# Kernel tuning notes

Measured on AMD Instinct MI355X. Metric: run time of the kernel, lower is better.

The kernel has to match this reference:

```python
import jax, jax.numpy as jnp
import numpy as np

NUM_GRAPHS = 256


def _gcn_norm(edge_index, num_nodes):
    # Add self-loops and compute symmetric normalization coeffs (PyG gcn_norm).
    loops = jnp.arange(num_nodes, dtype=edge_index.dtype)
    row = jnp.concatenate([edge_index[0], loops])  # source nodes
    col = jnp.concatenate([edge_index[1], loops])  # target nodes
    deg = jax.ops.segment_sum(jnp.ones_like(col, dtype=jnp.float32), col,
                              num_segments=num_nodes)
    dis = jnp.where(deg > 0, jax.lax.rsqrt(jnp.maximum(deg, 1.0)), 0.0)
    norm = dis[row] * dis[col]  # [E + N]
    return row, col, norm


def _gcn_conv(x, row, col, norm, W, b, num_nodes):
    h = x @ W                                        # [N, out] dense transform first
    msg = norm[:, None] * h[row]                     # gather + scale  [E+N, out]
    out = jax.ops.segment_sum(msg, col, num_segments=num_nodes)  # scatter-add
    return out + b


def setup_inputs() -> dict:
    key = jax.random.key(0)
    k = jax.random.split(key, 12)
    N, E, F_IN, H = 100000, 1600000, 64, 64
    x = jax.random.normal(k[0], (N, F_IN), dtype=jnp.float32)
    edge_index = jax.random.randint(k[1], (2, E), 0, N, dtype=jnp.int64)
    batch_index = jnp.sort(jax.random.randint(k[2], (N,), 0, NUM_GRAPHS, dtype=jnp.int64))
    s = 1.0 / np.sqrt(F_IN)
    W1 = jax.random.uniform(k[3], (F_IN, H), minval=-s, maxval=s, dtype=jnp.float32)
    b1 = jnp.zeros((H,), dtype=jnp.float32)
    W2 = jax.random.uniform(k[4], (H, H), minval=-s, maxval=s, dtype=jnp.float32)
    b2 = jnp.zeros((H,), dtype=jnp.float32)
    Wl1 = jax.random.uniform(k[5], (H, H // 2), minval=-s, maxval=s, dtype=jnp.float32)
    bl1 = jax.random.uniform(k[6], (H // 2,), minval=-s, maxval=s, dtype=jnp.float32)
    Wl2 = jax.random.uniform(k[7], (H // 2, 2), minval=-s, maxval=s, dtype=jnp.float32)
    bl2 = jax.random.uniform(k[8], (2,), minval=-s, maxval=s, dtype=jnp.float32)
    return {"x": x, "edge_index": edge_index, "batch_index": batch_index,
            "W1": W1, "b1": b1, "W2": W2, "b2": b2,
            "Wl1": Wl1, "bl1": bl1, "Wl2": Wl2, "bl2": bl2}


def reference(x, edge_index, batch_index, W1, b1, W2, b2, Wl1, bl1, Wl2, bl2):
    N = x.shape[0]
    row, col, norm = _gcn_norm(edge_index, N)
    h = jax.nn.relu(_gcn_conv(x, row, col, norm, W1, b1, N))
    h = jax.nn.relu(_gcn_conv(h, row, col, norm, W2, b2, N))
    # global mean pool over batch_index
    sums = jax.ops.segment_sum(h, batch_index, num_segments=NUM_GRAPHS)
    cnts = jax.ops.segment_sum(jnp.ones((N,), dtype=h.dtype), batch_index,
                               num_segments=NUM_GRAPHS)
    g = sums / jnp.maximum(cnts, 1.0)[:, None]       # [G, H]
    g = jax.nn.relu(g @ Wl1 + bl1)                    # dropout is identity in eval
    logits = g @ Wl2 + bl2
    return jax.nn.log_softmax(logits, axis=1)
```

## Files before the change

### kernel.cpp

```cpp
#include <hip/hip_runtime.h>
#include <hip/hip_fp8.h>
#include <cstdint>
#include <cstddef>


#define HF 64
#define BSH 8
#define BSZ 256
#define PCHUNK 4096
#define PADB 6144
#define CNTCLAMP (PADB - 4 * BSZ)
#define POISON 0xAAAAAAAAu

typedef unsigned u32;

__device__ __forceinline__ unsigned short f2bf(float x) {
    unsigned u = __float_as_uint(x);
    unsigned r = (u + 0x7fffu + ((u >> 16) & 1u)) >> 16;
    return (unsigned short)r;
}
__device__ __forceinline__ float bfl(u32 w) { return __uint_as_float(w << 16); }
__device__ __forceinline__ float bfh(u32 w) { return __uint_as_float(w & 0xffff0000u); }

__device__ __forceinline__ u32 pack_fp8x4(float a, float b, float c, float d) {
#if __has_builtin(__builtin_amdgcn_cvt_pk_fp8_f32)
    int v = 0;
    v = __builtin_amdgcn_cvt_pk_fp8_f32(a, b, v, false);
    v = __builtin_amdgcn_cvt_pk_fp8_f32(c, d, v, true);
    return (u32)v;
#else
    __hip_fp8_e4m3 fa(a), fb(b), fc(c), fd(d);
    return (u32)fa.__x | ((u32)fb.__x << 8) | ((u32)fc.__x << 16) | ((u32)fd.__x << 24);
#endif
}
__device__ __forceinline__ void acc_fp8x4(float4& acc, u32 w) {
#if __has_builtin(__builtin_amdgcn_cvt_pk_f32_fp8)
    typedef float v2f __attribute__((ext_vector_type(2)));
    v2f lo = __builtin_amdgcn_cvt_pk_f32_fp8((int)w, false);
    v2f hi = __builtin_amdgcn_cvt_pk_f32_fp8((int)w, true);
    acc.x += lo[0]; acc.y += lo[1]; acc.z += hi[0]; acc.w += hi[1];
#else
    __hip_fp8_e4m3 a, b, c, d;
    a.__x = (unsigned char)(w);       b.__x = (unsigned char)(w >> 8);
    c.__x = (unsigned char)(w >> 16); d.__x = (unsigned char)(w >> 24);
    acc.x += (float)a; acc.y += (float)b; acc.z += (float)c; acc.w += (float)d;
#endif
}

__global__ __launch_bounds__(256) void k_part(const int* __restrict__ rows,
                                              const int* __restrict__ cols,
                                              u32* __restrict__ gcurb,
                                              u32* __restrict__ part, int E) {
    __shared__ u32 hist[512];
    __shared__ u32 off[512];
    __shared__ u32 obase[512];
    __shared__ u32 cur[512];
    __shared__ u32 sc[256];
    __shared__ u32 stage[PCHUNK];
    __shared__ unsigned short sbk[PCHUNK];
    const int tid = threadIdx.x;
    const int e0  = blockIdx.x * PCHUNK;
    u32 er[16], ec[16];

    hist[tid] = 0; hist[tid + 256] = 0;
    __syncthreads();
#pragma unroll
    for (int j = 0; j < 16; ++j) {
        int e = e0 + j * 256 + tid;
        if (e < E) {
            ec[j] = (u32)cols[e];
            er[j] = (u32)rows[e];
            atomicAdd(&hist[ec[j] >> BSH], 1u);
        } else ec[j] = 0xFFFFFFFFu;
    }
    __syncthreads();
    u32 c0 = hist[2 * tid], c1 = hist[2 * tid + 1];
    u32 s = c0 + c1;
    sc[tid] = s;
    __syncthreads();
    for (int o = 1; o < 256; o <<= 1) {
        u32 t = (tid >= o) ? sc[tid - o] : 0u;
        __syncthreads();
        sc[tid] += t;
        __syncthreads();
    }
    u32 ex = sc[tid] - s;
    off[2 * tid] = ex;          cur[2 * tid] = ex;
    off[2 * tid + 1] = ex + c0; cur[2 * tid + 1] = ex + c0;
    obase[2 * tid]     = c0 ? (atomicAdd(&gcurb[2 * tid], c0) - POISON) : 0u;
    obase[2 * tid + 1] = c1 ? (atomicAdd(&gcurb[2 * tid + 1], c1) - POISON) : 0u;
    __syncthreads();
#pragma unroll
    for (int j = 0; j < 16; ++j) {
        if (ec[j] != 0xFFFFFFFFu) {
            u32 bk  = ec[j] >> BSH;
            u32 pos = atomicAdd(&cur[bk], 1u);
            stage[pos] = ((ec[j] & (BSZ - 1)) << 17) | er[j];
            sbk[pos]   = (unsigned short)bk;
        }
    }
    __syncthreads();
    const int total = (e0 + PCHUNK <= E) ? PCHUNK : (E - e0);
    for (int i = tid; i < total; i += 256) {
        u32 bk = sbk[i];
        u32 pb = obase[bk] + ((u32)i - off[bk]);
        if (pb < PADB)
            part[(size_t)bk * PADB + pb] = stage[i];
    }
}

__global__ __launch_bounds__(256) void k_place2(const u32* __restrict__ gcurb,
                                                const u32* __restrict__ part,
                                                const float* __restrict__ x,
                                                u32* __restrict__ rowptr,
                                                float* __restrict__ dis,
                                                u32* __restrict__ s08,
                                                u32* __restrict__ h18,
                                                int* __restrict__ eidx,
                                                int N, float S0) {
    __shared__ u32 cnt_[256];
    __shared__ u32 off_[257];
    __shared__ u32 sc[256];
    __shared__ u32 cur[256];
    __shared__ u32 outb[PADB];
    const int tid = threadIdx.x;
    const int b   = blockIdx.x;
    const int n0  = b << BSH;
    const u32 base = (u32)b * PADB;
    u32 cntB = gcurb[b] - POISON; if (cntB > CNTCLAMP) cntB = CNTCLAMP;

    if (b == 0 && tid < 16) {
        s08[(size_t)N * 16 + tid] = 0u;
        h18[(size_t)N * 16 + tid] = 0u;
    }

    cnt_[tid] = 0;
    __syncthreads();
    for (u32 i = tid; i < cntB; i += 256)
        atomicAdd(&cnt_[part[base + i] >> 17], 1u);
    __syncthreads();
    u32 v  = cnt_[tid];
    bool live = (n0 + tid) < N;
    u32 vs = v + 1u;
    u32 p  = live ? ((vs + 3u) & ~3u) : 0u;
    sc[tid] = p;
    __syncthreads();
    for (int o = 1; o < 256; o <<= 1) {
        u32 t = (tid >= o) ? sc[tid - o] : 0u;
        __syncthreads();
        sc[tid] += t;
        __syncthreads();
    }
    u32 ex = sc[tid] - p;
    off_[tid] = ex; cur[tid] = ex;
    if (tid == 255) off_[256] = sc[255];
    __syncthreads();
    const u32 cntP = off_[256];
    if (live) {
        u32 dg = vs; if (dg > 1023u) dg = 1023u;
        rowptr[n0 + tid] = (base + ex) | (dg << 22);
        dis[n0 + tid]    = rsqrtf(1.0f + (float)v);
    }
    {
        int nmax = min(256, N - n0);
        for (int idx = tid; idx < nmax * 16; idx += 256) {
            int nl = idx >> 4, f4 = idx & 15;
            float d  = S0 * rsqrtf(1.0f + (float)cnt_[nl]);
            float4 xv = ((const float4*)(x + (size_t)(n0 + nl) * HF))[f4];
            s08[(size_t)(n0 + nl) * 16 + f4] =
                pack_fp8x4(d * xv.x, d * xv.y, d * xv.z, d * xv.w);
        }
    }
    for (u32 i = tid; i < cntP; i += 256) outb[i] = (u32)N;
    __syncthreads();
    for (u32 i = tid; i < cntB; i += 256) {
        u32 pv  = part[base + i];
        u32 pos = atomicAdd(&cur[pv >> 17], 1u);
        outb[pos] = pv & 0x1FFFFu;
    }
    __syncthreads();
    if (live) outb[cur[tid]] = (u32)tid;
    __syncthreads();
    for (u32 i = tid; i < cntP; i += 256)
        eidx[base + i] = (int)outb[i];
}

template <int OUTFP8>
__global__ __launch_bounds__(256, 4) void k_gtrans(const u32* __restrict__ rowptr,
                                                   const int* __restrict__ eidx,
                                                   const u32* __restrict__ hs8,
                                                   const float* __restrict__ W,
                                                   const float* __restrict__ dis,
                                                   const float* __restrict__ bias,
                                                   void* __restrict__ OUTp, int N,
                                                   float invS, float outS) {
    __shared__ float ws[64 * 64];
    __shared__ float xs[64 * 68];
    const int tid  = threadIdx.x;
    const int row0 = blockIdx.x * 64;

#pragma unroll
    for (int i = 0; i < 4; ++i) {
        int idx4 = i * 256 + tid;
        *(float4*)&ws[idx4 * 4] = ((const float4*)W)[idx4];
    }

    const int qq = tid >> 4;
    const int f4 = tid & 15;
#pragma unroll 1
    for (int j = 0; j < 4; ++j) {
        const int n = row0 + qq * 4 + j;
        float4 acc = float4{0.f, 0.f, 0.f, 0.f};
        if (n < N) {
            u32 rp    = rowptr[n];
            u32 start = rp & 0x3FFFFFu;
            int ngr   = (int)(((rp >> 22) + 3u) >> 2);
            const uint4* eb = (const uint4*)(eidx + start);
            int g = 0;
            for (; g + 1 < ngr; g += 2) {
                uint4 ea = eb[g];
                uint4 eb2 = eb[g + 1];
                u32 wa0 = hs8[(size_t)ea.x * 16 + f4];
                u32 wa1 = hs8[(size_t)ea.y * 16 + f4];
                u32 wa2 = hs8[(size_t)ea.z * 16 + f4];
                u32 wa3 = hs8[(size_t)ea.w * 16 + f4];
                u32 wb0 = hs8[(size_t)eb2.x * 16 + f4];
                u32 wb1 = hs8[(size_t)eb2.y * 16 + f4];
                u32 wb2 = hs8[(size_t)eb2.z * 16 + f4];
                u32 wb3 = hs8[(size_t)eb2.w * 16 + f4];
                acc_fp8x4(acc, wa0); acc_fp8x4(acc, wa1);
                acc_fp8x4(acc, wa2); acc_fp8x4(acc, wa3);
                acc_fp8x4(acc, wb0); acc_fp8x4(acc, wb1);
                acc_fp8x4(acc, wb2); acc_fp8x4(acc, wb3);
            }
            if (g < ngr) {
                uint4 ea = eb[g];
                u32 w0 = hs8[(size_t)ea.x * 16 + f4];
                u32 w1 = hs8[(size_t)ea.y * 16 + f4];
                u32 w2 = hs8[(size_t)ea.z * 16 + f4];
                u32 w3 = hs8[(size_t)ea.w * 16 + f4];
                acc_fp8x4(acc, w0); acc_fp8x4(acc, w1);
                acc_fp8x4(acc, w2); acc_fp8x4(acc, w3);
            }
        }
        *(float4*)&xs[(qq * 4 + j) * 68 + f4 * 4] = acc;
    }
    __syncthreads();

    const int rg = tid >> 4;
    const int cg = tid & 15;
    float4 a0 = float4{0.f, 0.f, 0.f, 0.f};
    float4 a1 = a0, a2 = a0, a3 = a0;

#pragma unroll 8
    for (int k = 0; k < 64; ++k) {
        float4 wv = *(float4*)&ws[k * 64 + cg * 4];
        float  x0 = xs[(rg * 4 + 0) * 68 + k];
        float  x1 = xs[(rg * 4 + 1) * 68 + k];
        float  x2 = xs[(rg * 4 + 2) * 68 + k];
        float  x3 = xs[(rg * 4 + 3) * 68 + k];
        a0.x += x0 * wv.x; a0.y += x0 * wv.y; a0.z += x0 * wv.z; a0.w += x0 * wv.w;
        a1.x += x1 * wv.x; a1.y += x1 * wv.y; a1.z += x1 * wv.z; a1.w += x1 * wv.w;
        a2.x += x2 * wv.x; a2.y += x2 * wv.y; a2.z += x2 * wv.z; a2.w += x2 * wv.w;
        a3.x += x3 * wv.x; a3.y += x3 * wv.y; a3.z += x3 * wv.z; a3.w += x3 * wv.w;
    }

    float4 bv = ((const float4*)bias)[cg];
    float4 accs[4] = {a0, a1, a2, a3};
#pragma unroll
    for (int j = 0; j < 4; ++j) {
        int row = row0 + rg * 4 + j;
        if (row < N) {
            float d  = dis[row];
            float dd = d * invS;
            float4 a = accs[j];
            a.x = fmaxf(dd * a.x + bv.x, 0.f);
            a.y = fmaxf(dd * a.y + bv.y, 0.f);
            a.z = fmaxf(dd * a.z + bv.z, 0.f);
            a.w = fmaxf(dd * a.w + bv.w, 0.f);
            if (OUTFP8) {
                float so = d * outS;
                ((u32*)OUTp)[(size_t)row * 16 + cg] =
                    pack_fp8x4(so * a.x, so * a.y, so * a.z, so * a.w);
            } else {
                ushort4 pk;
                pk.x = f2bf(a.x); pk.y = f2bf(a.y);
                pk.z = f2bf(a.z); pk.w = f2bf(a.w);
                *(ushort4*)&((unsigned short*)OUTp)[(size_t)row * HF + cg * 4] = pk;
            }
        }
    }
}

__device__ __forceinline__ int lower_bound(const int* __restrict__ a, int n, int key) {
    int lo = 0, hi = n;
    while (lo < hi) { int mid = (lo + hi) >> 1; if (a[mid] < key) lo = mid + 1; else hi = mid; }
    return lo;
}

__global__ __launch_bounds__(256) void k_poolhead(const u32* __restrict__ h2,
                                                  const int* __restrict__ batch,
                                                  const float* __restrict__ Wl1,
                                                  const float* __restrict__ bl1,
                                                  const float* __restrict__ Wl2,
                                                  const float* __restrict__ bl2,
                                                  float* __restrict__ out, int N) {
    __shared__ float red[4][64];
    __shared__ float gm[64];
    const int g    = blockIdx.x;
    const int lane = threadIdx.x & 63;
    const int w    = threadIdx.x >> 6;
    int s = lower_bound(batch, N, g);
    int e = lower_bound(batch, N, g + 1);
    float acc = 0.f;
    for (int n = s + w; n < e; n += 4) {
        u32 wv = h2[(size_t)n * 32 + (lane >> 1)];
        acc += (lane & 1) ? bfh(wv) : bfl(wv);
    }
    red[w][lane] = acc;
    __syncthreads();
    if (w == 0) {
        float t = red[0][lane] + red[1][lane] + red[2][lane] + red[3][lane];
        gm[lane] = t / fmaxf((float)(e - s), 1.0f);
    }
    __syncthreads();
    if (w == 0 && lane < 32) {
        float a = bl1[lane];
#pragma unroll
        for (int k = 0; k < 64; ++k) a += gm[k] * Wl1[k * 32 + lane];
        a = fmaxf(a, 0.f);
        float l0 = a * Wl2[2 * lane];
        float l1 = a * Wl2[2 * lane + 1];
#pragma unroll
        for (int o = 1; o < 32; o <<= 1) {
            l0 += __shfl_xor(l0, o);
            l1 += __shfl_xor(l1, o);
        }
        if (lane == 0) {
            l0 += bl2[0]; l1 += bl2[1];
            float m   = fmaxf(l0, l1);
            float lse = m + logf(expf(l0 - m) + expf(l1 - m));
            out[2 * g]     = l0 - lse;
            out[2 * g + 1] = l1 - lse;
        }
    }
}

extern "C" void kernel_launch(void* const* d_in, const int* in_sizes, int n_in,
                              void* d_out, int out_size, void* d_ws, size_t ws_size,
                              hipStream_t stream) {
    const float* x   = (const float*)d_in[0];
    const int*   ei  = (const int*)d_in[1];
    const int*   bi  = (const int*)d_in[2];
    const float* W1  = (const float*)d_in[3];
    const float* b1  = (const float*)d_in[4];
    const float* W2  = (const float*)d_in[5];
    const float* b2  = (const float*)d_in[6];
    const float* Wl1 = (const float*)d_in[7];
    const float* bl1 = (const float*)d_in[8];
    const float* Wl2 = (const float*)d_in[9];
    const float* bl2 = (const float*)d_in[10];
    float* out = (float*)d_out;

    const int N = in_sizes[0] / HF;
    const int E = in_sizes[1] / 2;
    const int* rows = ei;
    const int* cols = ei + E;
    const int NB = (N + BSZ - 1) / BSZ;
    const size_t EP = (size_t)NB * PADB;

    const float S0 = 4.0f, S1 = 16.0f;

    float* ws = (float*)d_ws;
    size_t o = 0;
    float* dis    = ws + o; o += ((size_t)N + 63) / 64 * 64;
    u32*   A8     = (u32*)(ws + o); o += (size_t)(N + 1) * 16;
    u32*   B8     = (u32*)(ws + o); o += (size_t)(N + 1) * 16;
    unsigned short* Cbf = (unsigned short*)(ws + o); o += (size_t)N * 32;
    u32*   rowptr = (u32*)(ws + o); o += ((size_t)N + 63) / 64 * 64;
    u32*   part   = (u32*)(ws + o); o += EP;
    int*   eidx   = (int*)(ws + o); o += EP;
    u32*   gcurb  = (u32*)(ws + o); o += 512;

    const int tb = (N + 63) / 64;

    k_part<<<(E + PCHUNK - 1) / PCHUNK, 256, 0, stream>>>(rows, cols, gcurb, part, E);
    k_place2<<<NB, 256, 0, stream>>>(gcurb, part, x, rowptr, dis, A8, B8, eidx, N, S0);

    k_gtrans<1><<<tb, 256, 0, stream>>>(rowptr, eidx, A8, W1, dis, b1, (void*)B8,
                                        N, 1.0f / S0, S1);
    k_gtrans<0><<<tb, 256, 0, stream>>>(rowptr, eidx, B8, W2, dis, b2, (void*)Cbf,
                                        N, 1.0f / S1, 0.f);

    k_poolhead<<<256, 256, 0, stream>>>((const u32*)Cbf, bi, Wl1, bl1, Wl2, bl2, out, N);
}
```

Before: 249.3 us.

## Split gather across half-waves, store aggregated rows as bf16, split pooling across blocks

The gather in k_gtrans now has two 16-lane groups process alternate edge-groups of the same node and combine their partial sums with a shuffle. The aggregated rows are stored in shared memory as packed bf16, which roughly halves that buffer and lets launch bounds rise from 4 to 6 blocks per CU. Mean pooling is split over four blocks per graph using atomic adds into a zeroed buffer, and a separate small head kernel finishes the MLP. The aim is more memory-level parallelism and occupancy. In exchange there is bf16 rounding before the dense transform, float atomics, and one extra kernel launch.

```diff
diff --git a/kernel.cpp b/kernel.cpp
--- a/kernel.cpp
+++ b/kernel.cpp
@@ -11,6 +11,7 @@
 #define PADB 6144
 #define CNTCLAMP (PADB - 4 * BSZ)
 #define POISON 0xAAAAAAAAu
+#define NG 256
 
 typedef unsigned u32;
 
@@ -117,6 +118,7 @@
                                                 u32* __restrict__ s08,
                                                 u32* __restrict__ h18,
                                                 int* __restrict__ eidx,
+                                                float* __restrict__ gm,
                                                 int N, float S0) {
     __shared__ u32 cnt_[256];
     __shared__ u32 off_[257];
@@ -133,6 +135,9 @@
         s08[(size_t)N * 16 + tid] = 0u;
         h18[(size_t)N * 16 + tid] = 0u;
     }
+    if (b == 0) {
+        for (int i = tid; i < NG * HF; i += 256) gm[i] = 0.f;
+    }
 
     cnt_[tid] = 0;
     __syncthreads();
@@ -186,7 +191,7 @@
 }
 
 template <int OUTFP8>
-__global__ __launch_bounds__(256, 4) void k_gtrans(const u32* __restrict__ rowptr,
+__global__ __launch_bounds__(256, 6) void k_gtrans(const u32* __restrict__ rowptr,
                                                    const int* __restrict__ eidx,
                                                    const u32* __restrict__ hs8,
                                                    const float* __restrict__ W,
@@ -195,7 +200,7 @@
                                                    void* __restrict__ OUTp, int N,
                                                    float invS, float outS) {
     __shared__ float ws[64 * 64];
-    __shared__ float xs[64 * 68];
+    __shared__ u32 xs2[64 * 34];
     const int tid  = threadIdx.x;
     const int row0 = blockIdx.x * 64;
 
@@ -205,45 +210,42 @@
         *(float4*)&ws[idx4 * 4] = ((const float4*)W)[idx4];
     }
 
-    const int qq = tid >> 4;
-    const int f4 = tid & 15;
+    const int wv   = tid >> 6;
+    const int lane = tid & 63;
+    const int h    = lane >> 5;
+    const int qh   = (lane >> 4) & 1;
+    const int f4   = lane & 15;
 #pragma unroll 1
-    for (int j = 0; j < 4; ++j) {
-        const int n = row0 + qq * 4 + j;
+    for (int p = 0; p < 8; ++p) {
+        const int nl = wv * 16 + 2 * p + h;
+        const int n  = row0 + nl;
         float4 acc = float4{0.f, 0.f, 0.f, 0.f};
         if (n < N) {
             u32 rp    = rowptr[n];
             u32 start = rp & 0x3FFFFFu;
             int ngr   = (int)(((rp >> 22) + 3u) >> 2);
             const uint4* eb = (const uint4*)(eidx + start);
-            int g = 0;
-            for (; g + 1 < ngr; g += 2) {
-                uint4 ea = eb[g];
-                uint4 eb2 = eb[g + 1];
-                u32 wa0 = hs8[(size_t)ea.x * 16 + f4];
-                u32 wa1 = hs8[(size_t)ea.y * 16 + f4];
-                u32 wa2 = hs8[(size_t)ea.z * 16 + f4];
-                u32 wa3 = hs8[(size_t)ea.w * 16 + f4];
-                u32 wb0 = hs8[(size_t)eb2.x * 16 + f4];
-                u32 wb1 = hs8[(size_t)eb2.y * 16 + f4];
-                u32 wb2 = hs8[(size_t)eb2.z * 16 + f4];
-                u32 wb3 = hs8[(size_t)eb2.w * 16 + f4];
-                acc_fp8x4(acc, wa0); acc_fp8x4(acc, wa1);
-                acc_fp8x4(acc, wa2); acc_fp8x4(acc, wa3);
-                acc_fp8x4(acc, wb0); acc_fp8x4(acc, wb1);
-                acc_fp8x4(acc, wb2); acc_fp8x4(acc, wb3);
-            }
-            if (g < ngr) {
-                uint4 ea = eb[g];
-                u32 w0 = hs8[(size_t)ea.x * 16 + f4];
-                u32 w1 = hs8[(size_t)ea.y * 16 + f4];
-                u32 w2 = hs8[(size_t)ea.z * 16 + f4];
-                u32 w3 = hs8[(size_t)ea.w * 16 + f4];
+#pragma unroll 1
+            for (int g = qh; g < ngr; g += 2) {
+                uint4 e4 = eb[g];
+                u32 w0 = hs8[(size_t)e4.x * 16 + f4];
+                u32 w1 = hs8[(size_t)e4.y * 16 + f4];
+                u32 w2 = hs8[(size_t)e4.z * 16 + f4];
+                u32 w3 = hs8[(size_t)e4.w * 16 + f4];
                 acc_fp8x4(acc, w0); acc_fp8x4(acc, w1);
                 acc_fp8x4(acc, w2); acc_fp8x4(acc, w3);
             }
         }
-        *(float4*)&xs[(qq * 4 + j) * 68 + f4 * 4] = acc;
+        acc.x += __shfl_xor(acc.x, 16);
+        acc.y += __shfl_xor(acc.y, 16);
+        acc.z += __shfl_xor(acc.z, 16);
+        acc.w += __shfl_xor(acc.w, 16);
+        if (qh == 0) {
+            u32 lo = (u32)f2bf(acc.x) | ((u32)f2bf(acc.y) << 16);
+            u32 hi = (u32)f2bf(acc.z) | ((u32)f2bf(acc.w) << 16);
+            xs2[nl * 34 + f4 * 2]     = lo;
+            xs2[nl * 34 + f4 * 2 + 1] = hi;
+        }
     }
     __syncthreads();
 
@@ -252,17 +254,26 @@
     float4 a0 = float4{0.f, 0.f, 0.f, 0.f};
     float4 a1 = a0, a2 = a0, a3 = a0;
 
-#pragma unroll 8
-    for (int k = 0; k < 64; ++k) {
-        float4 wv = *(float4*)&ws[k * 64 + cg * 4];
-        float  x0 = xs[(rg * 4 + 0) * 68 + k];
-        float  x1 = xs[(rg * 4 + 1) * 68 + k];
-        float  x2 = xs[(rg * 4 + 2) * 68 + k];
-        float  x3 = xs[(rg * 4 + 3) * 68 + k];
-        a0.x += x0 * wv.x; a0.y += x0 * wv.y; a0.z += x0 * wv.z; a0.w += x0 * wv.w;
-        a1.x += x1 * wv.x; a1.y += x1 * wv.y; a1.z += x1 * wv.z; a1.w += x1 * wv.w;
-        a2.x += x2 * wv.x; a2.y += x2 * wv.y; a2.z += x2 * wv.z; a2.w += x2 * wv.w;
-        a3.x += x3 * wv.x; a3.y += x3 * wv.y; a3.z += x3 * wv.z; a3.w += x3 * wv.w;
+#pragma unroll 4
+    for (int k2 = 0; k2 < 32; ++k2) {
+        float4 wv0 = *(float4*)&ws[(2 * k2)     * 64 + cg * 4];
+        float4 wv1 = *(float4*)&ws[(2 * k2 + 1) * 64 + cg * 4];
+        u32 p0 = xs2[(rg * 4 + 0) * 34 + k2];
+        u32 p1 = xs2[(rg * 4 + 1) * 34 + k2];
+        u32 p2 = xs2[(rg * 4 + 2) * 34 + k2];
+        u32 p3 = xs2[(rg * 4 + 3) * 34 + k2];
+        float x0e = bfl(p0), x0o = bfh(p0);
+        float x1e = bfl(p1), x1o = bfh(p1);
+        float x2e = bfl(p2), x2o = bfh(p2);
+        float x3e = bfl(p3), x3o = bfh(p3);
+        a0.x += x0e * wv0.x; a0.y += x0e * wv0.y; a0.z += x0e * wv0.z; a0.w += x0e * wv0.w;
+        a1.x += x1e * wv0.x; a1.y += x1e * wv0.y; a1.z += x1e * wv0.z; a1.w += x1e * wv0.w;
+        a2.x += x2e * wv0.x; a2.y += x2e * wv0.y; a2.z += x2e * wv0.z; a2.w += x2e * wv0.w;
+        a3.x += x3e * wv0.x; a3.y += x3e * wv0.y; a3.z += x3e * wv0.z; a3.w += x3e * wv0.w;
+        a0.x += x0o * wv1.x; a0.y += x0o * wv1.y; a0.z += x0o * wv1.z; a0.w += x0o * wv1.w;
+        a1.x += x1o * wv1.x; a1.y += x1o * wv1.y; a1.z += x1o * wv1.z; a1.w += x1o * wv1.w;
+        a2.x += x2o * wv1.x; a2.y += x2o * wv1.y; a2.z += x2o * wv1.z; a2.w += x2o * wv1.w;
+        a3.x += x3o * wv1.x; a3.y += x3o * wv1.y; a3.z += x3o * wv1.z; a3.w += x3o * wv1.w;
     }
 
     float4 bv = ((const float4*)bias)[cg];
@@ -298,22 +309,21 @@
     return lo;
 }
 
-__global__ __launch_bounds__(256) void k_poolhead(const u32* __restrict__ h2,
-                                                  const int* __restrict__ batch,
-                                                  const float* __restrict__ Wl1,
-                                                  const float* __restrict__ bl1,
-                                                  const float* __restrict__ Wl2,
-                                                  const float* __restrict__ bl2,
-                                                  float* __restrict__ out, int N) {
+__global__ __launch_bounds__(256) void k_pool(const u32* __restrict__ h2,
+                                              const int* __restrict__ batch,
+                                              float* __restrict__ gm, int N) {
     __shared__ float red[4][64];
-    __shared__ float gm[64];
-    const int g    = blockIdx.x;
+    const int g    = blockIdx.x >> 2;
+    const int sl   = blockIdx.x & 3;
     const int lane = threadIdx.x & 63;
     const int w    = threadIdx.x >> 6;
     int s = lower_bound(batch, N, g);
     int e = lower_bound(batch, N, g + 1);
+    int len = e - s;
+    int q0 = s + ((len * sl) >> 2);
+    int q1 = s + ((len * (sl + 1)) >> 2);
     float acc = 0.f;
-    for (int n = s + w; n < e; n += 4) {
+    for (int n = q0 + w; n < q1; n += 4) {
         u32 wv = h2[(size_t)n * 32 + (lane >> 1)];
         acc += (lane & 1) ? bfh(wv) : bfl(wv);
     }
@@ -321,13 +331,28 @@
     __syncthreads();
     if (w == 0) {
         float t = red[0][lane] + red[1][lane] + red[2][lane] + red[3][lane];
-        gm[lane] = t / fmaxf((float)(e - s), 1.0f);
-    }
-    __syncthreads();
-    if (w == 0 && lane < 32) {
+        atomicAdd(&gm[g * HF + lane], t);
+    }
+}
+
+__global__ __launch_bounds__(64) void k_head(const float* __restrict__ gm,
+                                             const int* __restrict__ batch,
+                                             const float* __restrict__ Wl1,
+                                             const float* __restrict__ bl1,
+                                             const float* __restrict__ Wl2,
+                                             const float* __restrict__ bl2,
+                                             float* __restrict__ out, int N) {
+    __shared__ float gml[64];
+    const int g    = blockIdx.x;
+    const int lane = threadIdx.x;
+    int s = lower_bound(batch, N, g);
+    int e = lower_bound(batch, N, g + 1);
+    gml[lane] = gm[g * HF + lane] / fmaxf((float)(e - s), 1.0f);
+    __syncthreads();
+    if (lane < 32) {
         float a = bl1[lane];
 #pragma unroll
-        for (int k = 0; k < 64; ++k) a += gm[k] * Wl1[k * 32 + lane];
+        for (int k = 0; k < 64; ++k) a += gml[k] * Wl1[k * 32 + lane];
         a = fmaxf(a, 0.f);
         float l0 = a * Wl2[2 * lane];
         float l1 = a * Wl2[2 * lane + 1];
@@ -381,16 +406,18 @@
     u32*   part   = (u32*)(ws + o); o += EP;
     int*   eidx   = (int*)(ws + o); o += EP;
     u32*   gcurb  = (u32*)(ws + o); o += 512;
+    float* gm     = ws + o; o += (size_t)NG * HF;
 
     const int tb = (N + 63) / 64;
 
     k_part<<<(E + PCHUNK - 1) / PCHUNK, 256, 0, stream>>>(rows, cols, gcurb, part, E);
-    k_place2<<<NB, 256, 0, stream>>>(gcurb, part, x, rowptr, dis, A8, B8, eidx, N, S0);
+    k_place2<<<NB, 256, 0, stream>>>(gcurb, part, x, rowptr, dis, A8, B8, eidx, gm, N, S0);
 
     k_gtrans<1><<<tb, 256, 0, stream>>>(rowptr, eidx, A8, W1, dis, b1, (void*)B8,
                                         N, 1.0f / S0, S1);
     k_gtrans<0><<<tb, 256, 0, stream>>>(rowptr, eidx, B8, W2, dis, b2, (void*)Cbf,
                                         N, 1.0f / S1, 0.f);
 
-    k_poolhead<<<256, 256, 0, stream>>>((const u32*)Cbf, bi, Wl1, bl1, Wl2, bl2, out, N);
-}
+    k_pool<<<NG * 4, 256, 0, stream>>>((const u32*)Cbf, bi, gm, N);
+    k_head<<<NG, 64, 0, stream>>>(gm, bi, Wl1, bl1, Wl2, bl2, out, N);
+}
```

Measured after the change: 263.7 us. 1.06x slower.
